# Performance work log

Hardware: AMD Instinct MI355X
Metric: run time of the kernel (lower is better)

## Reference

```python
import jax, jax.numpy as jnp
import numpy as np

B, S, D, H = 2, 2048, 1024, 16
HD = D // H  # head size 64

def setup_inputs() -> dict:
    key = jax.random.key(0)
    ks = jax.random.split(key, 7)
    sc = 1.0 / np.sqrt(D)
    return {
        "batch_data": jax.random.normal(ks[0], (B, S, D), dtype=jnp.float32),
        "Wq": jax.random.normal(ks[1], (D, D), dtype=jnp.float32) * sc,
        "bq": jnp.zeros((D,), dtype=jnp.float32),
        "Wk": jax.random.normal(ks[2], (D, D), dtype=jnp.float32) * sc,
        "bk": jnp.zeros((D,), dtype=jnp.float32),
        "Wv": jax.random.normal(ks[3], (D, D), dtype=jnp.float32) * sc,
        "bv": jnp.zeros((D,), dtype=jnp.float32),
    }

def _split_heads(x):
    # [B,S,D] -> [B,H,S,HD]
    b, s, _ = x.shape
    return x.reshape(b, s, H, HD).transpose(0, 2, 1, 3)

def reference(batch_data, Wq, bq, Wk, bk, Wv, bv):
    q = _split_heads(batch_data @ Wq + bq)
    k = _split_heads(batch_data @ Wk + bk)
    v = _split_heads(batch_data @ Wv + bv)
    scores = jnp.einsum('bhqd,bhkd->bhqk', q, k) / jnp.sqrt(jnp.float32(HD))
    probs = jax.nn.softmax(scores, axis=-1)
    ctx = jnp.einsum('bhqk,bhkd->bhqd', probs, v)  # [B,H,S,HD]
    ctx = ctx.transpose(0, 2, 1, 3).reshape(batch_data.shape[0], batch_data.shape[1], D)
    return jnp.mean(ctx, axis=1)  # mean pool over sequence -> [B,D]
```

## Files before the change

kernel.cpp:

```cpp
#include <hip/hip_runtime.h>
#include <hip/hip_bf16.h>
#include <stdint.h>

#define B_  2
#define S_  2048
#define D_  1024
#define H_  16
#define HD_ 64

typedef __attribute__((ext_vector_type(8)))  __bf16 bf16x8;
typedef __attribute__((ext_vector_type(4)))  __bf16 bf16x4;
typedef __attribute__((ext_vector_type(2)))  __bf16 bf16x2;
typedef __attribute__((ext_vector_type(4)))  short  s16x4;
typedef __attribute__((ext_vector_type(8)))  short  s16x8;
typedef __attribute__((ext_vector_type(2)))  float  f32x2;
typedef __attribute__((ext_vector_type(4)))  float  f32x4;
typedef __attribute__((ext_vector_type(16))) float  f32x16;
typedef __attribute__((ext_vector_type(4)))  uint32_t u32x4;

#define QSCALE 0.18033688011112042f

__device__ __forceinline__ void gload16(const void* g, void* l) {
  __builtin_amdgcn_global_load_lds(
      (__attribute__((address_space(1))) void*)(uintptr_t)g,
      (__attribute__((address_space(3))) void*)(uintptr_t)l,
      16, 0, 0);
}

__device__ __forceinline__ bf16x8 cat8(s16x4 a, s16x4 b) {
  return __builtin_bit_cast(
      bf16x8, (s16x8)__builtin_shufflevector(a, b, 0, 1, 2, 3, 4, 5, 6, 7));
}


__global__ __launch_bounds__(256) void prep(
    const float* __restrict__ x, const float* __restrict__ wq,
    const float* __restrict__ wk, const float* __restrict__ wv,
    __bf16* __restrict__ xb, __bf16* __restrict__ wt, float* __restrict__ out) {
  __shared__ float tile[32][33];
  const int t = threadIdx.x;
  const int bx = blockIdx.x;
  if (bx < 4096) {
    int i = bx * 256 + t;
    float4 v = ((const float4*)x)[i];
    bf16x4 o;
    o[0] = (__bf16)v.x; o[1] = (__bf16)v.y; o[2] = (__bf16)v.z; o[3] = (__bf16)v.w;
    ((bf16x4*)xb)[i] = o;
  } else if (bx < 7168) {
    int tb = bx - 4096;
    int z = tb >> 10;
    int rem = tb & 1023;
    int n0 = (rem & 31) * 32, k0 = (rem >> 5) * 32;
    const float* w = (z == 0) ? wq : (z == 1 ? wk : wv);
    __bf16* o = wt + (size_t)z * D_ * D_;
    int tx = t & 31, ty = t >> 5;
    for (int i = 0; i < 4; ++i)
      tile[ty + 8 * i][tx] = w[(size_t)(k0 + ty + 8 * i) * D_ + n0 + tx];
    __syncthreads();
    for (int i = 0; i < 4; ++i)
      o[(size_t)(n0 + ty + 8 * i) * D_ + k0 + tx] = (__bf16)tile[tx][ty + 8 * i];
  } else {
    float4* o4 = (float4*)out;
    float4 z4 = {0.f, 0.f, 0.f, 0.f};
    o4[t] = z4;
    o4[t + 256] = z4;
  }
}

__global__ __launch_bounds__(256, 3) void gemm_qkv(
    const __bf16* __restrict__ xb, const __bf16* __restrict__ wt,
    const float* __restrict__ bq, const float* __restrict__ bk,
    const float* __restrict__ bv, __bf16* __restrict__ qh,
    __bf16* __restrict__ kh, __bf16* __restrict__ vt) {
  constexpr int K = 1024;
  constexpr int NIT = K / 32;
  __shared__ __attribute__((aligned(16))) __bf16 lA[2][128 * 32];
  __shared__ __attribute__((aligned(16))) __bf16 lB[2][128 * 32];

  const int z = blockIdx.z;
  const __bf16* w = wt + (size_t)z * K * D_;
  const float* bias = (z == 0) ? bq : (z == 1 ? bk : bv);
  const int t = threadIdx.x;
  const int lane = t & 63;
  const int wid = t >> 6;
  const int quad = lane >> 4;
  const int col = lane & 15;
  const int m0 = blockIdx.x * 128;
  const int n0 = blockIdx.y * 128;
  const int wr = (wid >> 1) * 64;
  const int wc = (wid & 1) * 64;

  const int sr0 = t >> 2;
  const int gc = (t & 3) ^ ((t >> 2) & 3);

  auto stage = [&](int kt, int buf) {
    gload16(xb + (size_t)(m0 + sr0) * K + kt * 32 + gc * 8,
            (char*)&lA[buf][0] + t * 16);
    gload16(xb + (size_t)(m0 + 64 + sr0) * K + kt * 32 + gc * 8,
            (char*)&lA[buf][0] + 4096 + t * 16);
    gload16(w + (size_t)(n0 + sr0) * K + kt * 32 + gc * 8,
            (char*)&lB[buf][0] + t * 16);
    gload16(w + (size_t)(n0 + 64 + sr0) * K + kt * 32 + gc * 8,
            (char*)&lB[buf][0] + 4096 + t * 16);
  };

  f32x4 acc[4][4] = {};

  stage(0, 0);

  if (z < 2) {
    for (int kt = 0; kt < NIT; ++kt) {
      const int cur = kt & 1;
      __syncthreads();
      if (kt + 1 < NIT) stage(kt + 1, cur ^ 1);
      bf16x8 fw[4], fx[4];
      for (int i = 0; i < 4; ++i) {
        int n = wr + i * 16 + col;
        int sl = quad ^ (n & 3);
        fw[i] = *(const bf16x8*)((const char*)&lB[cur][0] + n * 64 + sl * 16);
      }
      for (int j = 0; j < 4; ++j) {
        int m = wc + j * 16 + col;
        int sl = quad ^ (m & 3);
        fx[j] = *(const bf16x8*)((const char*)&lA[cur][0] + m * 64 + sl * 16);
      }
      for (int i = 0; i < 4; ++i)
        for (int j = 0; j < 4; ++j)
          acc[i][j] = __builtin_amdgcn_mfma_f32_16x16x32_bf16(
              fw[i], fx[j], acc[i][j], 0, 0, 0);
    }
    const float scale = (z == 0) ? QSCALE : 1.0f;
    __bf16* dst = (z == 0) ? qh : kh;
    for (int i = 0; i < 4; ++i) {
      int gnb = n0 + wr + i * 16 + quad * 4;
      float4 bi = *(const float4*)(bias + gnb);
      int h = gnb >> 6, hd = gnb & 63;
      for (int j = 0; j < 4; ++j) {
        int gm = m0 + wc + j * 16 + col;
        int b = gm >> 11, s = gm & 2047;
        bf16x4 pk;
        pk[0] = (__bf16)((acc[i][j][0] + bi.x) * scale);
        pk[1] = (__bf16)((acc[i][j][1] + bi.y) * scale);
        pk[2] = (__bf16)((acc[i][j][2] + bi.z) * scale);
        pk[3] = (__bf16)((acc[i][j][3] + bi.w) * scale);
        *(bf16x4*)(dst + ((size_t)(b * H_ + h) * S_ + s) * HD_ + hd) = pk;
      }
    }
  } else {
    for (int kt = 0; kt < NIT; ++kt) {
      const int cur = kt & 1;
      __syncthreads();
      if (kt + 1 < NIT) stage(kt + 1, cur ^ 1);
      bf16x8 fx[4], fw[4];
      for (int i = 0; i < 4; ++i) {
        int m = wr + i * 16 + col;
        int sl = quad ^ (m & 3);
        fx[i] = *(const bf16x8*)((const char*)&lA[cur][0] + m * 64 + sl * 16);
      }
      for (int j = 0; j < 4; ++j) {
        int n = wc + j * 16 + col;
        int sl = quad ^ (n & 3);
        fw[j] = *(const bf16x8*)((const char*)&lB[cur][0] + n * 64 + sl * 16);
      }
      for (int i = 0; i < 4; ++i)
        for (int j = 0; j < 4; ++j)
          acc[i][j] = __builtin_amdgcn_mfma_f32_16x16x32_bf16(
              fx[i], fw[j], acc[i][j], 0, 0, 0);
    }
    for (int i = 0; i < 4; ++i) {
      int gmb = m0 + wr + i * 16 + quad * 4;
      int b = gmb >> 11, s = gmb & 2047;
      for (int j = 0; j < 4; ++j) {
        int gn = n0 + wc + j * 16 + col;
        int h = gn >> 6, hd = gn & 63;
        float bi = bias[gn];
        bf16x4 pk;
        pk[0] = (__bf16)(acc[i][j][0] + bi);
        pk[1] = (__bf16)(acc[i][j][1] + bi);
        pk[2] = (__bf16)(acc[i][j][2] + bi);
        pk[3] = (__bf16)(acc[i][j][3] + bi);
        *(bf16x4*)(vt + ((size_t)(b * H_ + h) * HD_ + hd) * S_ + s) = pk;
      }
    }
  }
}

__global__ __launch_bounds__(256, 2) void attn1(
    const __bf16* __restrict__ qh, const __bf16* __restrict__ kh,
    const __bf16* __restrict__ vt, __bf16* __restrict__ po,
    float* __restrict__ pl) {
  __shared__ __attribute__((aligned(16))) __bf16 lK[2][64 * 64];
  __shared__ __attribute__((aligned(16))) __bf16 lV[2][64 * 64];

  const int t = threadIdx.x;
  const int lane = t & 63;
  const int half = lane >> 5;
  const int q31 = lane & 31;
  const int bh = blockIdx.x;
  const int kc = blockIdx.z;
  const int q0w = blockIdx.y * 256 + (t >> 6) * 64;

  const __bf16* qbase = qh + (size_t)bh * S_ * HD_;
  const __bf16* kbase = kh + (size_t)bh * S_ * HD_;
  const __bf16* vbase = vt + (size_t)bh * HD_ * S_;

  bf16x8 aq[2][4];
  for (int qt = 0; qt < 2; ++qt)
    for (int ks = 0; ks < 4; ++ks)
      aq[qt][ks] = *(const bf16x8*)(qbase +
          (size_t)(q0w + qt * 32 + q31) * HD_ + ks * 16 + half * 8);

  f32x16 o[2][2] = {};
  f32x2 ls[2] = {{0.f, 0.f}, {0.f, 0.f}};

  const int srow = t >> 3;
  const int sgc = (t & 7) ^ (srow & 7);

  const __bf16* kp  = kbase + (size_t)(kc * 1024 + srow) * HD_ + sgc * 8;
  const __bf16* kp2 = kp + 32 * HD_;
  const __bf16* vp  = vbase + (size_t)srow * S_ + kc * 1024 + sgc * 8;
  const __bf16* vp2 = vp + 32 * S_;
  char* lk0 = (char*)&lK[0][0] + t * 16;
  char* lv0 = (char*)&lV[0][0] + t * 16;

  auto stage = [&](int buf) {
    char* lk = lk0 + (buf << 13);
    char* lv = lv0 + (buf << 13);
    gload16(kp,  lk);
    gload16(kp2, lk + 4096);
    gload16(vp,  lv);
    gload16(vp2, lv + 4096);
    kp += 64 * HD_; kp2 += 64 * HD_;
    vp += 64;       vp2 += 64;
  };

  stage(0);

#pragma unroll 2
  for (int kt0 = 0; kt0 < 16; ++kt0) {
    const int cur = kt0 & 1;
    __syncthreads();
    if (kt0 + 1 < 16) stage(cur ^ 1);

    bf16x8 fk[2][4];
    s16x4  fv[2][2][4];
#pragma unroll
    for (int st = 0; st < 2; ++st) {
      const int row = st * 32 + q31;
#pragma unroll
      for (int ks = 0; ks < 4; ++ks) {
        int pos = (2 * ks + half) ^ (row & 7);
        fk[st][ks] = *(const bf16x8*)((const char*)&lK[cur][0] + row * 128 + pos * 16);
      }
    }
#pragma unroll
    for (int st = 0; st < 2; ++st)
#pragma unroll
      for (int hdt = 0; hdt < 2; ++hdt) {
        const int rowv = hdt * 32 + q31;
#pragma unroll
        for (int g = 0; g < 4; ++g) {
          int pos = (4 * st + g) ^ (rowv & 7);
          fv[st][hdt][g] = *(const s16x4*)((const char*)&lV[cur][0] + rowv * 128 +
                                           pos * 16 + half * 8);
        }
      }

#pragma unroll
    for (int st = 0; st < 2; ++st) {
      f32x16 sc0 = {}, sc1 = {};
#pragma unroll
      for (int ks = 0; ks < 4; ++ks) {
        sc0 = __builtin_amdgcn_mfma_f32_32x32x16_bf16(fk[st][ks], aq[0][ks], sc0, 0, 0, 0);
        sc1 = __builtin_amdgcn_mfma_f32_32x32x16_bf16(fk[st][ks], aq[1][ks], sc1, 0, 0, 0);
      }

      uint32_t pk0[8], pk1[8];
#pragma unroll
      for (int p = 0; p < 8; ++p) {
        float ea = __builtin_amdgcn_exp2f(sc0[2 * p]);
        float eb = __builtin_amdgcn_exp2f(sc0[2 * p + 1]);
        f32x2 e2 = {ea, eb};
        ls[0] += e2;
        uint32_t au = __builtin_bit_cast(uint32_t, ea) + 0x8000u;
        uint32_t bu = __builtin_bit_cast(uint32_t, eb) + 0x8000u;
        pk0[p] = __builtin_amdgcn_perm(bu, au, 0x07060302u);
      }
#pragma unroll
      for (int p = 0; p < 8; ++p) {
        float ea = __builtin_amdgcn_exp2f(sc1[2 * p]);
        float eb = __builtin_amdgcn_exp2f(sc1[2 * p + 1]);
        f32x2 e2 = {ea, eb};
        ls[1] += e2;
        uint32_t au = __builtin_bit_cast(uint32_t, ea) + 0x8000u;
        uint32_t bu = __builtin_bit_cast(uint32_t, eb) + 0x8000u;
        pk1[p] = __builtin_amdgcn_perm(bu, au, 0x07060302u);
      }

      u32x4 w;
      w[0] = pk0[0]; w[1] = pk0[1]; w[2] = pk0[2]; w[3] = pk0[3];
      bf16x8 fp0a = __builtin_bit_cast(bf16x8, w);
      w[0] = pk0[4]; w[1] = pk0[5]; w[2] = pk0[6]; w[3] = pk0[7];
      bf16x8 fp0b = __builtin_bit_cast(bf16x8, w);
      w[0] = pk1[0]; w[1] = pk1[1]; w[2] = pk1[2]; w[3] = pk1[3];
      bf16x8 fp1a = __builtin_bit_cast(bf16x8, w);
      w[0] = pk1[4]; w[1] = pk1[5]; w[2] = pk1[6]; w[3] = pk1[7];
      bf16x8 fp1b = __builtin_bit_cast(bf16x8, w);

#pragma unroll
      for (int hdt = 0; hdt < 2; ++hdt) {
        bf16x8 av0 = cat8(fv[st][hdt][0], fv[st][hdt][1]);
        bf16x8 av1 = cat8(fv[st][hdt][2], fv[st][hdt][3]);
        o[0][hdt] = __builtin_amdgcn_mfma_f32_32x32x16_bf16(av0, fp0a, o[0][hdt], 0, 0, 0);
        o[1][hdt] = __builtin_amdgcn_mfma_f32_32x32x16_bf16(av0, fp1a, o[1][hdt], 0, 0, 0);
        o[0][hdt] = __builtin_amdgcn_mfma_f32_32x32x16_bf16(av1, fp0b, o[0][hdt], 0, 0, 0);
        o[1][hdt] = __builtin_amdgcn_mfma_f32_32x32x16_bf16(av1, fp1b, o[1][hdt], 0, 0, 0);
      }
    }
  }

  const size_t slab = (size_t)(kc * 32 + bh) * S_;
  for (int qt = 0; qt < 2; ++qt) {
    float lq = ls[qt].x + ls[qt].y;
    float ltot = lq + __shfl_xor(lq, 32);
    const int qrow = q0w + qt * 32 + q31;
    if (half == 0) pl[slab + qrow] = ltot;
    for (int hdt = 0; hdt < 2; ++hdt)
      for (int rq = 0; rq < 4; ++rq) {
        bf16x4 pk;
        pk[0] = (__bf16)o[qt][hdt][rq * 4 + 0];
        pk[1] = (__bf16)o[qt][hdt][rq * 4 + 1];
        pk[2] = (__bf16)o[qt][hdt][rq * 4 + 2];
        pk[3] = (__bf16)o[qt][hdt][rq * 4 + 3];
        *(bf16x4*)(po + (slab + qrow) * HD_ + hdt * 32 + rq * 8 + half * 4) = pk;
      }
  }
}

__global__ __launch_bounds__(256) void attn2(const __bf16* __restrict__ po,
                                             const float* __restrict__ pl,
                                             float* __restrict__ out) {
  __shared__ float red[256];
  const int t = threadIdx.x;
  const int hd = t & 63;
  const int rgrp = t >> 6;
  const int bh = blockIdx.y;
  const int r0 = blockIdx.x * 64 + rgrp * 16;
  const size_t s0 = (size_t)bh * S_;
  const size_t s1 = (size_t)(32 + bh) * S_;
  float acc = 0.f;
#pragma unroll 4
  for (int i = 0; i < 16; ++i) {
    int row = r0 + i;
    float l = pl[s0 + row] + pl[s1 + row];
    float v = (float)po[(s0 + row) * HD_ + hd] +
              (float)po[(s1 + row) * HD_ + hd];
    acc += v / l;
  }
  red[t] = acc;
  __syncthreads();
  if (t < 64) {
    float s = red[t] + red[t + 64] + red[t + 128] + red[t + 192];
    atomicAdd(out + (size_t)(bh >> 4) * D_ + (bh & 15) * HD_ + hd,
              s * (1.0f / S_));
  }
}

extern "C" void kernel_launch(void* const* d_in, const int* in_sizes, int n_in,
                              void* d_out, int out_size, void* d_ws, size_t ws_size,
                              hipStream_t stream) {
  const float* x  = (const float*)d_in[0];
  const float* Wq = (const float*)d_in[1];
  const float* bq = (const float*)d_in[2];
  const float* Wk = (const float*)d_in[3];
  const float* bk = (const float*)d_in[4];
  const float* Wv = (const float*)d_in[5];
  const float* bv = (const float*)d_in[6];
  float* out = (float*)d_out;

  char* ws = (char*)d_ws;
  __bf16* qh = (__bf16*)(ws);
  __bf16* kh = (__bf16*)(ws + ((size_t)8  << 20));
  __bf16* vt = (__bf16*)(ws + ((size_t)16 << 20));
  __bf16* xb = (__bf16*)(ws + ((size_t)24 << 20));
  __bf16* wt = (__bf16*)(ws + ((size_t)32 << 20));
  __bf16* po = (__bf16*)(ws + ((size_t)24 << 20));
  float*  pl = (float*) (ws + ((size_t)40 << 20));

  prep<<<dim3(7169), dim3(256), 0, stream>>>(x, Wq, Wk, Wv, xb, wt, out);
  gemm_qkv<<<dim3(32, 8, 3), dim3(256), 0, stream>>>(xb, wt, bq, bk, bv, qh, kh, vt);
  attn1<<<dim3(B_ * H_, 8, 2), dim3(256), 0, stream>>>(qh, kh, vt, po, pl);
  attn2<<<dim3(32, B_ * H_), dim3(256), 0, stream>>>(po, pl, out);
}
```

Baseline: 164.9 us.

## Halve per-wave query tile in attention to double grid and occupancy

Each wave in attn1 now handles 32 query rows instead of 64. This halves the accumulator, Q-fragment and score registers, and launch bounds are raised to 4 blocks per CU. The grid doubles along the query axis (16 instead of 8 blocks), and K/V LDS fragment loads are interleaved per sub-tile to shorten live ranges. In exchange each K/V tile staged into LDS is reused by fewer queries, so global/LDS traffic per unit of MFMA work doubles.

Result: no change. 166.5 us (+0.9%).

```diff
diff --git a/kernel.cpp b/kernel.cpp
--- a/kernel.cpp
+++ b/kernel.cpp
@@ -10,7 +10,6 @@
 
 typedef __attribute__((ext_vector_type(8)))  __bf16 bf16x8;
 typedef __attribute__((ext_vector_type(4)))  __bf16 bf16x4;
-typedef __attribute__((ext_vector_type(2)))  __bf16 bf16x2;
 typedef __attribute__((ext_vector_type(4)))  short  s16x4;
 typedef __attribute__((ext_vector_type(8)))  short  s16x8;
 typedef __attribute__((ext_vector_type(2)))  float  f32x2;
@@ -185,7 +184,7 @@
   }
 }
 
-__global__ __launch_bounds__(256, 2) void attn1(
+__global__ __launch_bounds__(256, 4) void attn1(
     const __bf16* __restrict__ qh, const __bf16* __restrict__ kh,
     const __bf16* __restrict__ vt, __bf16* __restrict__ po,
     float* __restrict__ pl) {
@@ -198,20 +197,20 @@
   const int q31 = lane & 31;
   const int bh = blockIdx.x;
   const int kc = blockIdx.z;
-  const int q0w = blockIdx.y * 256 + (t >> 6) * 64;
+  const int q0w = blockIdx.y * 128 + (t >> 6) * 32;
 
   const __bf16* qbase = qh + (size_t)bh * S_ * HD_;
   const __bf16* kbase = kh + (size_t)bh * S_ * HD_;
   const __bf16* vbase = vt + (size_t)bh * HD_ * S_;
 
-  bf16x8 aq[2][4];
-  for (int qt = 0; qt < 2; ++qt)
-    for (int ks = 0; ks < 4; ++ks)
-      aq[qt][ks] = *(const bf16x8*)(qbase +
-          (size_t)(q0w + qt * 32 + q31) * HD_ + ks * 16 + half * 8);
-
-  f32x16 o[2][2] = {};
-  f32x2 ls[2] = {{0.f, 0.f}, {0.f, 0.f}};
+  bf16x8 aq[4];
+#pragma unroll
+  for (int ks = 0; ks < 4; ++ks)
+    aq[ks] = *(const bf16x8*)(qbase +
+        (size_t)(q0w + q31) * HD_ + ks * 16 + half * 8);
+
+  f32x16 o[2] = {};
+  f32x2 ls = {0.f, 0.f};
 
   const int srow = t >> 3;
   const int sgc = (t & 7) ^ (srow & 7);
@@ -242,99 +241,77 @@
     __syncthreads();
     if (kt0 + 1 < 16) stage(cur ^ 1);
 
-    bf16x8 fk[2][4];
-    s16x4  fv[2][2][4];
 #pragma unroll
     for (int st = 0; st < 2; ++st) {
+      bf16x8 fk[4];
       const int row = st * 32 + q31;
 #pragma unroll
       for (int ks = 0; ks < 4; ++ks) {
-        int pos = (2 * ks + half) ^ (row & 7);
-        fk[st][ks] = *(const bf16x8*)((const char*)&lK[cur][0] + row * 128 + pos * 16);
-      }
-    }
-#pragma unroll
-    for (int st = 0; st < 2; ++st)
+        int pos = (2 * ks + half) ^ (q31 & 7);
+        fk[ks] = *(const bf16x8*)((const char*)&lK[cur][0] + row * 128 + pos * 16);
+      }
+
+      f32x16 sc = {};
+#pragma unroll
+      for (int ks = 0; ks < 4; ++ks)
+        sc = __builtin_amdgcn_mfma_f32_32x32x16_bf16(fk[ks], aq[ks], sc, 0, 0, 0);
+
+      s16x4 fv[2][4];
 #pragma unroll
       for (int hdt = 0; hdt < 2; ++hdt) {
         const int rowv = hdt * 32 + q31;
 #pragma unroll
         for (int g = 0; g < 4; ++g) {
-          int pos = (4 * st + g) ^ (rowv & 7);
-          fv[st][hdt][g] = *(const s16x4*)((const char*)&lV[cur][0] + rowv * 128 +
-                                           pos * 16 + half * 8);
+          int pos = (4 * st + g) ^ (q31 & 7);
+          fv[hdt][g] = *(const s16x4*)((const char*)&lV[cur][0] + rowv * 128 +
+                                       pos * 16 + half * 8);
         }
       }
 
-#pragma unroll
-    for (int st = 0; st < 2; ++st) {
-      f32x16 sc0 = {}, sc1 = {};
-#pragma unroll
-      for (int ks = 0; ks < 4; ++ks) {
-        sc0 = __builtin_amdgcn_mfma_f32_32x32x16_bf16(fk[st][ks], aq[0][ks], sc0, 0, 0, 0);
-        sc1 = __builtin_amdgcn_mfma_f32_32x32x16_bf16(fk[st][ks], aq[1][ks], sc1, 0, 0, 0);
-      }
-
-      uint32_t pk0[8], pk1[8];
+      uint32_t pk[8];
 #pragma unroll
       for (int p = 0; p < 8; ++p) {
-        float ea = __builtin_amdgcn_exp2f(sc0[2 * p]);
-        float eb = __builtin_amdgcn_exp2f(sc0[2 * p + 1]);
+        float ea = __builtin_amdgcn_exp2f(sc[2 * p]);
+        float eb = __builtin_amdgcn_exp2f(sc[2 * p + 1]);
         f32x2 e2 = {ea, eb};
-        ls[0] += e2;
+        ls += e2;
         uint32_t au = __builtin_bit_cast(uint32_t, ea) + 0x8000u;
         uint32_t bu = __builtin_bit_cast(uint32_t, eb) + 0x8000u;
-        pk0[p] = __builtin_amdgcn_perm(bu, au, 0x07060302u);
-      }
-#pragma unroll
-      for (int p = 0; p < 8; ++p) {
-        float ea = __builtin_amdgcn_exp2f(sc1[2 * p]);
-        float eb = __builtin_amdgcn_exp2f(sc1[2 * p + 1]);
-        f32x2 e2 = {ea, eb};
-        ls[1] += e2;
-        uint32_t au = __builtin_bit_cast(uint32_t, ea) + 0x8000u;
-        uint32_t bu = __builtin_bit_cast(uint32_t, eb) + 0x8000u;
-        pk1[p] = __builtin_amdgcn_perm(bu, au, 0x07060302u);
+        pk[p] = __builtin_amdgcn_perm(bu, au, 0x07060302u);
       }
 
       u32x4 w;
-      w[0] = pk0[0]; w[1] = pk0[1]; w[2] = pk0[2]; w[3] = pk0[3];
-      bf16x8 fp0a = __builtin_bit_cast(bf16x8, w);
-      w[0] = pk0[4]; w[1] = pk0[5]; w[2] = pk0[6]; w[3] = pk0[7];
-      bf16x8 fp0b = __builtin_bit_cast(bf16x8, w);
-      w[0] = pk1[0]; w[1] = pk1[1]; w[2] = pk1[2]; w[3] = pk1[3];
-      bf16x8 fp1a = __builtin_bit_cast(bf16x8, w);
-      w[0] = pk1[4]; w[1] = pk1[5]; w[2] = pk1[6]; w[3] = pk1[7];
-      bf16x8 fp1b = __builtin_bit_cast(bf16x8, w);
+      w[0] = pk[0]; w[1] = pk[1]; w[2] = pk[2]; w[3] = pk[3];
+      bf16x8 fpa = __builtin_bit_cast(bf16x8, w);
+      w[0] = pk[4]; w[1] = pk[5]; w[2] = pk[6]; w[3] = pk[7];
+      bf16x8 fpb = __builtin_bit_cast(bf16x8, w);
 
 #pragma unroll
       for (int hdt = 0; hdt < 2; ++hdt) {
-        bf16x8 av0 = cat8(fv[st][hdt][0], fv[st][hdt][1]);
-        bf16x8 av1 = cat8(fv[st][hdt][2], fv[st][hdt][3]);
-        o[0][hdt] = __builtin_amdgcn_mfma_f32_32x32x16_bf16(av0, fp0a, o[0][hdt], 0, 0, 0);
-        o[1][hdt] = __builtin_amdgcn_mfma_f32_32x32x16_bf16(av0, fp1a, o[1][hdt], 0, 0, 0);
-        o[0][hdt] = __builtin_amdgcn_mfma_f32_32x32x16_bf16(av1, fp0b, o[0][hdt], 0, 0, 0);
-        o[1][hdt] = __builtin_amdgcn_mfma_f32_32x32x16_bf16(av1, fp1b, o[1][hdt], 0, 0, 0);
+        bf16x8 av0 = cat8(fv[hdt][0], fv[hdt][1]);
+        bf16x8 av1 = cat8(fv[hdt][2], fv[hdt][3]);
+        o[hdt] = __builtin_amdgcn_mfma_f32_32x32x16_bf16(av0, fpa, o[hdt], 0, 0, 0);
+        o[hdt] = __builtin_amdgcn_mfma_f32_32x32x16_bf16(av1, fpb, o[hdt], 0, 0, 0);
       }
     }
   }
 
   const size_t slab = (size_t)(kc * 32 + bh) * S_;
-  for (int qt = 0; qt < 2; ++qt) {
-    float lq = ls[qt].x + ls[qt].y;
-    float ltot = lq + __shfl_xor(lq, 32);
-    const int qrow = q0w + qt * 32 + q31;
-    if (half == 0) pl[slab + qrow] = ltot;
-    for (int hdt = 0; hdt < 2; ++hdt)
-      for (int rq = 0; rq < 4; ++rq) {
-        bf16x4 pk;
-        pk[0] = (__bf16)o[qt][hdt][rq * 4 + 0];
-        pk[1] = (__bf16)o[qt][hdt][rq * 4 + 1];
-        pk[2] = (__bf16)o[qt][hdt][rq * 4 + 2];
-        pk[3] = (__bf16)o[qt][hdt][rq * 4 + 3];
-        *(bf16x4*)(po + (slab + qrow) * HD_ + hdt * 32 + rq * 8 + half * 4) = pk;
-      }
-  }
+  float lq = ls.x + ls.y;
+  float ltot = lq + __shfl_xor(lq, 32);
+  const int qrow = q0w + q31;
+  if (half == 0) pl[slab + qrow] = ltot;
+#pragma unroll
+  for (int hdt = 0; hdt < 2; ++hdt)
+#pragma unroll
+    for (int rq = 0; rq < 4; ++rq) {
+      bf16x4 pk4;
+      pk4[0] = (__bf16)o[hdt][rq * 4 + 0];
+      pk4[1] = (__bf16)o[hdt][rq * 4 + 1];
+      pk4[2] = (__bf16)o[hdt][rq * 4 + 2];
+      pk4[3] = (__bf16)o[hdt][rq * 4 + 3];
+      *(bf16x4*)(po + (slab + qrow) * HD_ + hdt * 32 + rq * 8 + half * 4) = pk4;
+    }
 }
 
 __global__ __launch_bounds__(256) void attn2(const __bf16* __restrict__ po,
@@ -389,6 +366,6 @@
 
   prep<<<dim3(7169), dim3(256), 0, stream>>>(x, Wq, Wk, Wv, xb, wt, out);
   gemm_qkv<<<dim3(32, 8, 3), dim3(256), 0, stream>>>(xb, wt, bq, bk, bv, qh, kh, vt);
-  attn1<<<dim3(B_ * H_, 8, 2), dim3(256), 0, stream>>>(qh, kh, vt, po, pl);
+  attn1<<<dim3(B_ * H_, 16, 2), dim3(256), 0, stream>>>(qh, kh, vt, po, pl);
   attn2<<<dim3(32, B_ * H_), dim3(256), 0, stream>>>(po, pl, out);
 }
```
